# Kernel tuning notes

Hardware: AMD Instinct MI355X
Metric: run time of the kernel (lower is better)

Reference implementation:

```python
import jax, jax.numpy as jnp
import numpy as np

N_NODES = 50000
N_EDGES = 800000
D_IN = 8
D_MODEL = 128
N_CLASSES = 2


def gcn_conv(x, W, b, src, dst, n_nodes):
    # PyG GCNConv: h = x @ W; add self-loops; D^{-1/2} A D^{-1/2} aggregation; + bias
    h = x @ W  # [N, D]
    deg = jax.ops.segment_sum(jnp.ones(src.shape[0], h.dtype), dst, num_segments=n_nodes) + 1.0  # +1 self-loop
    dinv = jax.lax.rsqrt(deg)  # deg >= 1 always
    norm = dinv[src] * dinv[dst]  # [E]
    agg = jax.ops.segment_sum(h[src] * norm[:, None], dst, num_segments=n_nodes)
    agg = agg + h * (dinv * dinv)[:, None]  # self-loop term, norm_ii = dinv_i^2
    return agg + b


def setup_inputs() -> dict:
    key = jax.random.key(0)
    ks = jax.random.split(key, 10)
    x = jax.random.normal(ks[0], (N_NODES, D_IN), jnp.float32)
    edge_index = jax.random.randint(ks[1], (2, N_EDGES), 0, N_NODES, jnp.int64 if jax.config.jax_enable_x64 else jnp.int32)
    def glorot(k, shape):
        lim = np.sqrt(6.0 / (shape[0] + shape[1]))
        return jax.random.uniform(k, shape, jnp.float32, -lim, lim)
    return {
        "x": x,
        "edge_index": edge_index,
        "W1": glorot(ks[2], (D_IN, D_MODEL)),
        "b1": jnp.zeros((D_MODEL,), jnp.float32),
        "W2": glorot(ks[3], (D_MODEL, D_MODEL)),
        "b2": jnp.zeros((D_MODEL,), jnp.float32),
        "Wlin1": glorot(ks[4], (2 * D_MODEL, D_MODEL)),
        "blin1": jnp.zeros((D_MODEL,), jnp.float32),
        "Wfin": glorot(ks[5], (D_MODEL, N_CLASSES)),
        "bfin": jnp.zeros((N_CLASSES,), jnp.float32),
    }


def reference(x, edge_index, W1, b1, W2, b2, Wlin1, blin1, Wfin, bfin):
    src, dst = edge_index[0], edge_index[1]
    n = x.shape[0]
    h = jax.nn.relu(gcn_conv(x, W1, b1, src, dst, n))
    h = jax.nn.relu(gcn_conv(h, W2, b2, src, dst, n))
    xpair = jnp.concatenate((h[src], h[dst]), axis=1)  # [E, 2*D]
    xpair = jax.nn.relu(xpair @ Wlin1 + blin1)
    logits = xpair @ Wfin + bfin  # [E, C]
    return jax.nn.log_softmax(logits, axis=1)
```

## Files before the change

### kernel.cpp

```cpp
#include <hip/hip_runtime.h>
#include <stdint.h>
#include <math.h>

#define D 128

typedef unsigned short u16;
typedef __attribute__((ext_vector_type(8))) short bf16x8;
typedef __attribute__((ext_vector_type(4))) float f32x4;
typedef __attribute__((ext_vector_type(2))) float f32x2;

union BU { uint4 u; bf16x8 s; };

__device__ __forceinline__ unsigned f2bf_pk(float a, float b) {
    union { float f; unsigned u; } x, y; x.f = a; y.f = b;
    unsigned ra = x.u + 0x7FFF + ((x.u >> 16) & 1);
    unsigned rb = y.u + 0x7FFF + ((y.u >> 16) & 1);
    return (ra >> 16) | (rb & 0xFFFF0000u);
}
__device__ __forceinline__ u16 f2bf(float f) {
    union { float f; unsigned u; } x; x.f = f;
    unsigned r = x.u + 0x7FFF + ((x.u >> 16) & 1);
    return (u16)(r >> 16);
}
__device__ __forceinline__ f32x2 bf2f2v(unsigned u) {
    union { unsigned w[2]; f32x2 v; } t;
    t.w[0] = u << 16; t.w[1] = u & 0xFFFF0000u;
    return t.v;
}
__device__ __forceinline__ f32x2 vmax0(f32x2 a) {
    return __builtin_elementwise_max(a, (f32x2)(0.f));
}
__device__ __forceinline__ int padded4(int deg) {
    return (deg + 3) & ~3;
}


__global__ __launch_bounds__(256) void k_degree8(const int* __restrict__ dst, int E,
                                                 int* __restrict__ hist8, int* __restrict__ rank, int N) {
    int i = blockIdx.x * 256 + threadIdx.x;
    int copy = blockIdx.x & 7;
    int E4 = E >> 2;
    if (i < E4) {
        int4 d = ((const int4*)dst)[i];
        int* h = hist8 + copy * N;
        int4 rk;
        rk.x = atomicAdd(&h[d.x], 1);
        rk.y = atomicAdd(&h[d.y], 1);
        rk.z = atomicAdd(&h[d.z], 1);
        rk.w = atomicAdd(&h[d.w], 1);
        ((int4*)rank)[i] = rk;
    }
    if (i == 0) {
        for (int j = E4 * 4; j < E; ++j) rank[j] = atomicAdd(&hist8[dst[j]], 1);
    }
}

__global__ __launch_bounds__(256) void k_xcdoff_bsum(int* __restrict__ hist8, int* __restrict__ degi,
                                                     float* __restrict__ dinv, int* __restrict__ bsum, int N) {
    __shared__ int ws[4];
    int t = threadIdx.x;
    int i = blockIdx.x * 256 + t;
    int pd = 0;
    if (i < N) {
        int run = 0;
#pragma unroll
        for (int j = 0; j < 8; ++j) {
            int c = hist8[j * N + i];
            hist8[j * N + i] = run;
            run += c;
        }
        degi[i] = run;
        dinv[i] = rsqrtf((float)run + 1.0f);
        pd = padded4(run);
    }
    int v = pd;
#pragma unroll
    for (int off = 1; off < 64; off <<= 1) v += __shfl_xor(v, off, 64);
    if ((t & 63) == 0) ws[t >> 6] = v;
    __syncthreads();
    if (t == 0) bsum[blockIdx.x] = ws[0] + ws[1] + ws[2] + ws[3];
}

__global__ __launch_bounds__(1024) void k_boff_wprep(const int* __restrict__ bsum, int* __restrict__ boff,
                                                     int nb, int* __restrict__ prow, int N,
                                                     const float* __restrict__ W2, const float* __restrict__ Wlin,
                                                     unsigned* __restrict__ wswz) {
    int t = threadIdx.x;
    if (blockIdx.x == 0) {
        __shared__ int s[1024];
        s[t] = (t < nb) ? bsum[t] : 0;
        __syncthreads();
        for (int off = 1; off < 1024; off <<= 1) {
            int v = (t >= off) ? s[t - off] : 0;
            __syncthreads();
            s[t] += v;
            __syncthreads();
        }
        if (t < nb) boff[t] = (t == 0) ? 0 : s[t - 1];
        if (t == 0) prow[N] = s[1023];
    } else {
        int tid = (blockIdx.x - 1) * 1024 + t;
        int m = tid >> 13;
        int r = tid & 8191;
        int jp = r & 3;
        int lane = (r >> 2) & 63;
        int ct = (r >> 8) & 7;
        int kc = r >> 11;
        int k0 = kc * 32 + (lane >> 4) * 8 + 2 * jp;
        int n = ct * 16 + (lane & 15);
        const float* srcp = (m == 0) ? W2 : (Wlin + (m - 1) * 16384);
        wswz[tid] = f2bf_pk(srcp[k0 * 128 + n], srcp[(k0 + 1) * 128 + n]);
    }
}

__global__ __launch_bounds__(256) void k_scan_final(const int* __restrict__ degi, const int* __restrict__ boff,
                                                    int* __restrict__ prow, int N, int* __restrict__ hist8) {
    __shared__ int s[256];
    int t = threadIdx.x;
    int i = blockIdx.x * 256 + t;
    int pd = (i < N) ? padded4(degi[i]) : 0;
    s[t] = pd;
    __syncthreads();
    for (int off = 1; off < 256; off <<= 1) {
        int v = (t >= off) ? s[t - off] : 0;
        __syncthreads();
        s[t] += v;
        __syncthreads();
    }
    if (i < N) {
        int p = boff[blockIdx.x] + ((t == 0) ? 0 : s[t - 1]);
        prow[i] = p;
#pragma unroll
        for (int j = 0; j < 8; ++j) hist8[j * N + i] += p;
    }
}


__global__ __launch_bounds__(256) void k_scatter_fill_xform(
        const int* __restrict__ src, const int* __restrict__ dst, int E,
        const int* __restrict__ prow, const int* __restrict__ hist8, const int* __restrict__ rank,
        const int* __restrict__ degi,
        int* __restrict__ colsrc, int N, int eb4, int nb,
        const float* __restrict__ x, const float* __restrict__ W1,
        const float* __restrict__ dinv, unsigned* __restrict__ g) {
    __shared__ float Ws[8 * D];
    int t = threadIdx.x;
    int b = blockIdx.x;
    if (b < eb4) {
        int i = b * 256 + t;
        int copy = b & 7;
        int E4 = E >> 2;
        if (i < E4) {
            int4 d = ((const int4*)dst)[i];
            int4 s4 = ((const int4*)src)[i];
            int4 rk = ((const int4*)rank)[i];
            const int* h = hist8 + copy * N;
            colsrc[h[d.x] + rk.x] = s4.x;
            colsrc[h[d.y] + rk.y] = s4.y;
            colsrc[h[d.z] + rk.z] = s4.z;
            colsrc[h[d.w] + rk.w] = s4.w;
        }
        if (i == 0) {
            for (int j = E4 * 4; j < E; ++j)
                colsrc[hist8[dst[j]] + rank[j]] = src[j];
        }
    } else if (b < eb4 + nb) {
        int n = (b - eb4) * 256 + t;
        if (n < N) {
            int lo = prow[n];
            int deg = degi[n];
            int pd = padded4(deg);
            for (int j = deg; j < pd; ++j) colsrc[lo + j] = N;
        }
        if (b == eb4 && t == 0) {
            int P = prow[N];
            for (int j = 0; j < 16; ++j) colsrc[P + j] = N;
        }
    } else {
        int xb0 = b - eb4 - nb;
        for (int i = t; i < 8 * D; i += 256) Ws[i] = W1[i];
        __syncthreads();
        int node = xb0 * 4 + (t >> 6);
        int l = t & 63;
        if (node < N) {
            float s0 = 0.f, s1 = 0.f;
#pragma unroll
            for (int k = 0; k < 8; ++k) {
                float xv = x[node * 8 + k];
                s0 += xv * Ws[k * D + 2 * l];
                s1 += xv * Ws[k * D + 2 * l + 1];
            }
            float di = dinv[node];
            g[node * 64 + l] = f2bf_pk(s0 * di, s1 * di);
        }
        if (xb0 == 0 && t < 64) g[(size_t)N * 64 + t] = 0;
    }
}


#define HROW 136

template <bool DUAL>
__global__ __launch_bounds__(256) void k_aggemm(const uint4* __restrict__ g, const int* __restrict__ prow,
                                                const int* __restrict__ colsrc, const float* __restrict__ dinv,
                                                const float* __restrict__ biasH,
                                                const uint4* __restrict__ wB0, const uint4* __restrict__ wB1,
                                                const float* __restrict__ bias1,
                                                u16* __restrict__ out0, u16* __restrict__ out1, int N) {
    __shared__ u16 hs[16 * HROW];
    int t = threadIdx.x;
    int wv = t >> 6;
    int lane = t & 63;
    int sub = lane >> 4;
    int r = lane & 15;
    int base = blockIdx.x * 16;

    for (int nd = 0; nd < 4; ++nd) {
        int i = base + wv * 4 + nd;
        int lrow = wv * 4 + nd;
        if (i < N) {
            f32x2 acc2[4];
#pragma unroll
            for (int j = 0; j < 4; ++j) acc2[j] = (f32x2)(0.f);
            int lo = prow[i], hiP = prow[i + 1];
            int idx = lo + sub;
            int c0 = colsrc[idx];
            int c1 = (idx + 4 < hiP) ? colsrc[idx + 4] : N;
            int c2 = (idx + 8 < hiP) ? colsrc[idx + 8] : N;
            uint4 v0 = g[c0 * 16 + r];
            uint4 v1 = g[c1 * 16 + r];
            for (int k = lo; k < hiP; k += 4) {
                int c3 = (idx + 12 < hiP) ? colsrc[idx + 12] : N;
                uint4 v2 = g[c2 * 16 + r];
                acc2[0] += bf2f2v(v0.x);
                acc2[1] += bf2f2v(v0.y);
                acc2[2] += bf2f2v(v0.z);
                acc2[3] += bf2f2v(v0.w);
                v0 = v1; v1 = v2; c2 = c3; idx += 4;
            }
#pragma unroll
            for (int j = 0; j < 4; ++j) {
                acc2[j].x += __shfl_xor(acc2[j].x, 16, 64);
                acc2[j].y += __shfl_xor(acc2[j].y, 16, 64);
                acc2[j].x += __shfl_xor(acc2[j].x, 32, 64);
                acc2[j].y += __shfl_xor(acc2[j].y, 32, 64);
            }
            if (sub == 0) {
                uint4 sv = g[i * 16 + r];
                acc2[0] += bf2f2v(sv.x);
                acc2[1] += bf2f2v(sv.y);
                acc2[2] += bf2f2v(sv.z);
                acc2[3] += bf2f2v(sv.w);
                float di = dinv[i];
                float4 b0 = ((const float4*)biasH)[r * 2];
                float4 b1v = ((const float4*)biasH)[r * 2 + 1];
                float r0 = fmaxf(acc2[0].x * di + b0.x, 0.f);
                float r1 = fmaxf(acc2[0].y * di + b0.y, 0.f);
                float r2 = fmaxf(acc2[1].x * di + b0.z, 0.f);
                float r3 = fmaxf(acc2[1].y * di + b0.w, 0.f);
                float r4 = fmaxf(acc2[2].x * di + b1v.x, 0.f);
                float r5 = fmaxf(acc2[2].y * di + b1v.y, 0.f);
                float r6 = fmaxf(acc2[3].x * di + b1v.z, 0.f);
                float r7 = fmaxf(acc2[3].y * di + b1v.w, 0.f);
                uint4 o;
                o.x = f2bf_pk(r0, r1);
                o.y = f2bf_pk(r2, r3);
                o.z = f2bf_pk(r4, r5);
                o.w = f2bf_pk(r6, r7);
                *(uint4*)(hs + lrow * HROW + r * 8) = o;
            }
        } else if (sub == 0) {
            *(uint4*)(hs + lrow * HROW + r * 8) = make_uint4(0, 0, 0, 0);
        }
    }
    __syncthreads();

    int quad = lane >> 4;
    int l15 = lane & 15;
    int ct0 = wv * 2;

    f32x4 accA[2], accB[2];
#pragma unroll
    for (int q = 0; q < 2; ++q) { accA[q] = (f32x4){0.f, 0.f, 0.f, 0.f}; accB[q] = (f32x4){0.f, 0.f, 0.f, 0.f}; }

    const uint4* hrow = (const uint4*)(hs + l15 * HROW);
#pragma unroll
    for (int kc = 0; kc < 4; ++kc) {
        BU a; a.u = hrow[kc * 4 + quad];
#pragma unroll
        for (int q = 0; q < 2; ++q) {
            BU b0; b0.u = wB0[(kc * 8 + ct0 + q) * 64 + lane];
            accA[q] = __builtin_amdgcn_mfma_f32_16x16x32_bf16(a.s, b0.s, accA[q], 0, 0, 0);
            if (DUAL) {
                BU b1; b1.u = wB1[(kc * 8 + ct0 + q) * 64 + lane];
                accB[q] = __builtin_amdgcn_mfma_f32_16x16x32_bf16(a.s, b1.s, accB[q], 0, 0, 0);
            }
        }
    }
#pragma unroll
    for (int reg = 0; reg < 4; ++reg) {
        int node = base + quad * 4 + reg;
        if (node >= N) continue;
        float sc = DUAL ? 1.0f : dinv[node];
#pragma unroll
        for (int q = 0; q < 2; ++q) {
            int colj = (ct0 + q) * 16 + l15;
            out0[(size_t)node * 128 + colj] = f2bf(accA[q][reg] * sc);
            if (DUAL) out1[(size_t)node * 128 + colj] = f2bf(accB[q][reg] + bias1[colj]);
        }
    }
    if (blockIdx.x == 0 && t < 64) ((unsigned*)out0)[(size_t)N * 64 + t] = 0;
}


__global__ __launch_bounds__(256) void k_edge(const uint4* __restrict__ a, const uint4* __restrict__ c,
                                              const int* __restrict__ src, const int* __restrict__ dst,
                                              const float* __restrict__ Wfin, const float* __restrict__ bfin,
                                              float* __restrict__ out, int E) {
    int t = threadIdx.x;
    int g = t >> 4;
    int r = t & 15;
    int base = blockIdx.x * 64 + g * 4;

    f32x2 wd[4];
    const float4* wvp = (const float4*)Wfin;
#pragma unroll
    for (int q = 0; q < 4; ++q) {
        float4 m = wvp[r * 4 + q];
        wd[q] = (f32x2){m.x - m.y, m.z - m.w};
    }
    float bd = bfin[0] - bfin[1];

    int4 s4, d4;
    if (base + 3 < E) {
        s4 = ((const int4*)src)[blockIdx.x * 16 + g];
        d4 = ((const int4*)dst)[blockIdx.x * 16 + g];
    } else {
        int e0 = base, e1 = base + 1, e2 = base + 2, e3 = base + 3;
        s4.x = (e0 < E) ? src[e0] : 0; d4.x = (e0 < E) ? dst[e0] : 0;
        s4.y = (e1 < E) ? src[e1] : 0; d4.y = (e1 < E) ? dst[e1] : 0;
        s4.z = (e2 < E) ? src[e2] : 0; d4.z = (e2 < E) ? dst[e2] : 0;
        s4.w = (e3 < E) ? src[e3] : 0; d4.w = (e3 < E) ? dst[e3] : 0;
    }

    uint4 av[4], cv[4];
    av[0] = a[(size_t)s4.x * 16 + r];  cv[0] = c[(size_t)d4.x * 16 + r];
    av[1] = a[(size_t)s4.y * 16 + r];  cv[1] = c[(size_t)d4.y * 16 + r];
    av[2] = a[(size_t)s4.z * 16 + r];  cv[2] = c[(size_t)d4.z * 16 + r];
    av[3] = a[(size_t)s4.w * 16 + r];  cv[3] = c[(size_t)d4.w * 16 + r];

    float dl[4];
#pragma unroll
    for (int j = 0; j < 4; ++j) {
        f32x2 p = (f32x2)(0.f);
        f32x2 z;
        z = vmax0(bf2f2v(av[j].x) + bf2f2v(cv[j].x)); p += z * wd[0];
        z = vmax0(bf2f2v(av[j].y) + bf2f2v(cv[j].y)); p += z * wd[1];
        z = vmax0(bf2f2v(av[j].z) + bf2f2v(cv[j].z)); p += z * wd[2];
        z = vmax0(bf2f2v(av[j].w) + bf2f2v(cv[j].w)); p += z * wd[3];
        dl[j] = p.x + p.y;
    }
#pragma unroll
    for (int off = 1; off < 16; off <<= 1) {
#pragma unroll
        for (int j = 0; j < 4; ++j) dl[j] += __shfl_xor(dl[j], off, 64);
    }
    if (r == 0) {
        float o[8];
#pragma unroll
        for (int j = 0; j < 4; ++j) {
            float dlt = dl[j] + bd;
            float tn = -fabsf(dlt);
            float s = __logf(1.f + __expf(tn));
            o[2 * j]     = (dlt >= 0.f) ? -s : (dlt - s);
            o[2 * j + 1] = (dlt >= 0.f) ? (-dlt - s) : -s;
        }
        if (base + 3 < E) {
            float4* op = (float4*)(out + 2 * (size_t)base);
            op[0] = make_float4(o[0], o[1], o[2], o[3]);
            op[1] = make_float4(o[4], o[5], o[6], o[7]);
        } else {
#pragma unroll
            for (int j = 0; j < 4; ++j) {
                if (base + j < E)
                    *((float2*)(out + 2 * (size_t)(base + j))) = make_float2(o[2 * j], o[2 * j + 1]);
            }
        }
    }
}

extern "C" void kernel_launch(void* const* d_in, const int* in_sizes, int n_in,
                              void* d_out, int out_size, void* d_ws, size_t ws_size,
                              hipStream_t stream) {
    const float* x     = (const float*)d_in[0];
    const int*   ei    = (const int*)d_in[1];
    const float* W1    = (const float*)d_in[2];
    const float* b1    = (const float*)d_in[3];
    const float* W2    = (const float*)d_in[4];
    const float* b2    = (const float*)d_in[5];
    const float* Wlin1 = (const float*)d_in[6];
    const float* blin1 = (const float*)d_in[7];
    const float* Wfin  = (const float*)d_in[8];
    const float* bfin  = (const float*)d_in[9];
    float* out = (float*)d_out;

    int N = in_sizes[0] / 8;
    int E = in_sizes[1] / 2;
    const int* src = ei;
    const int* dst = ei + E;
    int nb = (N + 255) / 256;
    int eb4 = (E / 4 + 255) / 256;
    int xb = (N + 3) / 4;

    char* w = (char*)d_ws;
    int* hist8 = (int*)w;     w += (size_t)8 * N * 4;
    int* rank = (int*)w;      w += (size_t)E * 4;
    int* degi = (int*)w;      w += (size_t)N * 4;
    int* prow = (int*)w;      w += (size_t)(N + 1) * 4;
    float* dinv = (float*)w;  w += (size_t)N * 4;
    int* bsum = (int*)w;      w += (size_t)nb * 4;
    int* boff = (int*)w;      w += (size_t)nb * 4;
    w = (char*)(((uintptr_t)w + 255) & ~(uintptr_t)255);
    int* colsrc = (int*)w;    w += ((size_t)E + 8 * (size_t)N + 64) * 4;
    unsigned* wswz = (unsigned*)w; w += (size_t)3 * 8192 * 4;
    unsigned* bufG = (unsigned*)w; w += (size_t)(N + 1) * 64 * 4;
    unsigned* bufA = (unsigned*)w; w += (size_t)(N + 1) * 64 * 4;
    unsigned* bufC = (unsigned*)w; w += (size_t)N * 64 * 4;
    unsigned* bufG2 = (unsigned*)w; w += (size_t)(N + 1) * 64 * 4;

    hipMemsetAsync(hist8, 0, (size_t)8 * N * 4, stream);

    k_degree8<<<eb4, 256, 0, stream>>>(dst, E, hist8, rank, N);
    k_xcdoff_bsum<<<nb, 256, 0, stream>>>(hist8, degi, dinv, bsum, N);
    k_boff_wprep<<<25, 1024, 0, stream>>>(bsum, boff, nb, prow, N, W2, Wlin1, wswz);
    k_scan_final<<<nb, 256, 0, stream>>>(degi, boff, prow, N, hist8);
    k_scatter_fill_xform<<<eb4 + nb + xb, 256, 0, stream>>>(src, dst, E, prow, hist8, rank, degi,
                                                            colsrc, N, eb4, nb, x, W1, dinv, bufG);

    int ablocks = (N + 15) / 16;
    k_aggemm<false><<<ablocks, 256, 0, stream>>>((const uint4*)bufG, prow, colsrc, dinv, b1,
                                                 (const uint4*)wswz, nullptr, nullptr,
                                                 (u16*)bufG2, nullptr, N);
    k_aggemm<true><<<ablocks, 256, 0, stream>>>((const uint4*)bufG2, prow, colsrc, dinv, b2,
                                                (const uint4*)(wswz + 8192), (const uint4*)(wswz + 16384),
                                                blin1, (u16*)bufA, (u16*)bufC, N);

    k_edge<<<(E + 63) / 64, 256, 0, stream>>>((const uint4*)bufA, (const uint4*)bufC,
                                              src, dst, Wfin, bfin, out, E);
}
```

Measured before the change: 273.9 us.

## Aggregate 8-dim raw features before W1 transform in first GCN layer

Layer one now aggregates the dinv-scaled 8-wide input features over neighbors, and only then applies W1, bias and ReLU, followed by the W2 MFMA GEMM in the same kernel. Previously it gathered 128-wide bf16 rows. The prescaled features are written in the degree kernel, and the separate x@W1 transform blocks are dropped from the scatter kernel. This cuts gather traffic in the first aggregation roughly by a factor of eight and keeps the layer-1 math in fp32 before the bf16 cast. The cost is a small per-node 8x128 matmul done on scalar units.

Result: slower. 280.2 us (+2.3%).

```diff
diff --git a/kernel.cpp b/kernel.cpp
--- a/kernel.cpp
+++ b/kernel.cpp
@@ -56,7 +56,8 @@
 }
 
 __global__ __launch_bounds__(256) void k_xcdoff_bsum(int* __restrict__ hist8, int* __restrict__ degi,
-                                                     float* __restrict__ dinv, int* __restrict__ bsum, int N) {
+                                                     float* __restrict__ dinv, int* __restrict__ bsum, int N,
+                                                     const float* __restrict__ x, float* __restrict__ xs) {
     __shared__ int ws[4];
     int t = threadIdx.x;
     int i = blockIdx.x * 256 + t;
@@ -70,8 +71,19 @@
             run += c;
         }
         degi[i] = run;
-        dinv[i] = rsqrtf((float)run + 1.0f);
+        float dv = rsqrtf((float)run + 1.0f);
+        dinv[i] = dv;
+        const float4* xp = (const float4*)(x + (size_t)i * 8);
+        float4 a0 = xp[0], a1 = xp[1];
+        float4 w0 = make_float4(dv * a0.x, dv * a0.y, dv * a0.z, dv * a0.w);
+        float4 w1 = make_float4(dv * a1.x, dv * a1.y, dv * a1.z, dv * a1.w);
+        float4* xo = (float4*)(xs + (size_t)i * 8);
+        xo[0] = w0; xo[1] = w1;
         pd = padded4(run);
+    } else if (i == N) {
+        float4 z = make_float4(0.f, 0.f, 0.f, 0.f);
+        float4* xo = (float4*)(xs + (size_t)N * 8);
+        xo[0] = z; xo[1] = z;
     }
     int v = pd;
 #pragma unroll
@@ -136,21 +148,18 @@
 }
 
 
-__global__ __launch_bounds__(256) void k_scatter_fill_xform(
+__global__ __launch_bounds__(256) void k_scatter_fill(
         const int* __restrict__ src, const int* __restrict__ dst, int E,
         const int* __restrict__ prow, const int* __restrict__ hist8, const int* __restrict__ rank,
         const int* __restrict__ degi,
-        int* __restrict__ colsrc, int N, int eb4, int nb,
-        const float* __restrict__ x, const float* __restrict__ W1,
-        const float* __restrict__ dinv, unsigned* __restrict__ g) {
-    __shared__ float Ws[8 * D];
+        int* __restrict__ colsrc, int N, int eb4) {
     int t = threadIdx.x;
     int b = blockIdx.x;
     if (b < eb4) {
         int i = b * 256 + t;
-        int copy = b & 7;
         int E4 = E >> 2;
         if (i < E4) {
+            int copy = b & 7;
             int4 d = ((const int4*)dst)[i];
             int4 s4 = ((const int4*)src)[i];
             int4 rk = ((const int4*)rank)[i];
@@ -164,7 +173,7 @@
             for (int j = E4 * 4; j < E; ++j)
                 colsrc[hist8[dst[j]] + rank[j]] = src[j];
         }
-    } else if (b < eb4 + nb) {
+    } else {
         int n = (b - eb4) * 256 + t;
         if (n < N) {
             int lo = prow[n];
@@ -176,29 +185,119 @@
             int P = prow[N];
             for (int j = 0; j < 16; ++j) colsrc[P + j] = N;
         }
-    } else {
-        int xb0 = b - eb4 - nb;
-        for (int i = t; i < 8 * D; i += 256) Ws[i] = W1[i];
-        __syncthreads();
-        int node = xb0 * 4 + (t >> 6);
-        int l = t & 63;
-        if (node < N) {
-            float s0 = 0.f, s1 = 0.f;
-#pragma unroll
-            for (int k = 0; k < 8; ++k) {
-                float xv = x[node * 8 + k];
-                s0 += xv * Ws[k * D + 2 * l];
-                s1 += xv * Ws[k * D + 2 * l + 1];
+    }
+}
+
+#define HROW 136
+
+
+__global__ __launch_bounds__(256) void k_agg1gemm(
+        const float* __restrict__ xs, const int* __restrict__ prow,
+        const int* __restrict__ colsrc, const float* __restrict__ dinv,
+        const float* __restrict__ b1, const float* __restrict__ W1,
+        const uint4* __restrict__ wB0, u16* __restrict__ out0, int N) {
+    __shared__ float W1s[8 * 128];
+    __shared__ float b1s[128];
+    __shared__ float ys[16][8];
+    __shared__ u16 hs[16 * HROW];
+    int t = threadIdx.x;
+    int wv = t >> 6;
+    int lane = t & 63;
+    int sub = lane >> 4;
+    int r = lane & 15;
+    int base = blockIdx.x * 16;
+
+    for (int idx = t; idx < 8 * 128; idx += 256) W1s[idx] = W1[idx];
+    if (t < 128) b1s[t] = b1[t];
+
+    int i = base + wv * 4 + sub;
+    if (i < N) {
+        float acc[8];
+#pragma unroll
+        for (int f = 0; f < 8; ++f) acc[f] = 0.f;
+        int lo = prow[i], hiP = prow[i + 1];
+        for (int k = lo + r; k < hiP; k += 16) {
+            int cj = colsrc[k];
+            const float4* xr = (const float4*)(xs + (size_t)cj * 8);
+            float4 u0 = xr[0], u1 = xr[1];
+            acc[0] += u0.x; acc[1] += u0.y; acc[2] += u0.z; acc[3] += u0.w;
+            acc[4] += u1.x; acc[5] += u1.y; acc[6] += u1.z; acc[7] += u1.w;
+        }
+#pragma unroll
+        for (int off = 1; off < 16; off <<= 1) {
+#pragma unroll
+            for (int f = 0; f < 8; ++f) acc[f] += __shfl_xor(acc[f], off, 64);
+        }
+        const float4* xi = (const float4*)(xs + (size_t)i * 8);
+        float4 s0 = xi[0], s1 = xi[1];
+        float di = dinv[i];
+        acc[0] = di * (acc[0] + s0.x); acc[1] = di * (acc[1] + s0.y);
+        acc[2] = di * (acc[2] + s0.z); acc[3] = di * (acc[3] + s0.w);
+        acc[4] = di * (acc[4] + s1.x); acc[5] = di * (acc[5] + s1.y);
+        acc[6] = di * (acc[6] + s1.z); acc[7] = di * (acc[7] + s1.w);
+        if (r < 8) ys[wv * 4 + sub][r] = acc[r];
+    }
+    __syncthreads();
+
+    {
+        int node16 = t >> 4;
+        int cseg = (t & 15) * 8;
+        if (base + node16 < N) {
+            float yv[8];
+#pragma unroll
+            for (int f = 0; f < 8; ++f) yv[f] = ys[node16][f];
+            float o[8];
+#pragma unroll
+            for (int c = 0; c < 8; ++c) {
+                float s = b1s[cseg + c];
+#pragma unroll
+                for (int f = 0; f < 8; ++f) s += yv[f] * W1s[f * 128 + cseg + c];
+                o[c] = fmaxf(s, 0.f);
             }
-            float di = dinv[node];
-            g[node * 64 + l] = f2bf_pk(s0 * di, s1 * di);
-        }
-        if (xb0 == 0 && t < 64) g[(size_t)N * 64 + t] = 0;
-    }
-}
-
-
-#define HROW 136
+            uint4 ov;
+            ov.x = f2bf_pk(o[0], o[1]);
+            ov.y = f2bf_pk(o[2], o[3]);
+            ov.z = f2bf_pk(o[4], o[5]);
+            ov.w = f2bf_pk(o[6], o[7]);
+            *(uint4*)(hs + node16 * HROW + cseg) = ov;
+        } else {
+            *(uint4*)(hs + node16 * HROW + cseg) = make_uint4(0, 0, 0, 0);
+        }
+    }
+    __syncthreads();
+
+    int quad = lane >> 4;
+    int l15 = lane & 15;
+    int ct0 = wv * 2;
+
+    f32x4 accA[2];
+#pragma unroll
+    for (int q = 0; q < 2; ++q) accA[q] = (f32x4){0.f, 0.f, 0.f, 0.f};
+
+    const uint4* hrow = (const uint4*)(hs + l15 * HROW);
+#pragma unroll
+    for (int kc = 0; kc < 4; ++kc) {
+        BU a; a.u = hrow[kc * 4 + quad];
+#pragma unroll
+        for (int q = 0; q < 2; ++q) {
+            BU b0; b0.u = wB0[(kc * 8 + ct0 + q) * 64 + lane];
+            accA[q] = __builtin_amdgcn_mfma_f32_16x16x32_bf16(a.s, b0.s, accA[q], 0, 0, 0);
+        }
+    }
+#pragma unroll
+    for (int reg = 0; reg < 4; ++reg) {
+        int node = base + quad * 4 + reg;
+        if (node >= N) continue;
+        float sc = dinv[node];
+#pragma unroll
+        for (int q = 0; q < 2; ++q) {
+            int colj = (ct0 + q) * 16 + l15;
+            out0[(size_t)node * 128 + colj] = f2bf(accA[q][reg] * sc);
+        }
+    }
+    if (blockIdx.x == 0 && t < 64) ((unsigned*)out0)[(size_t)N * 64 + t] = 0;
+}
+
 
 template <bool DUAL>
 __global__ __launch_bounds__(256) void k_aggemm(const uint4* __restrict__ g, const int* __restrict__ prow,
@@ -410,7 +509,6 @@
     const int* dst = ei + E;
     int nb = (N + 255) / 256;
     int eb4 = (E / 4 + 255) / 256;
-    int xb = (N + 3) / 4;
 
     char* w = (char*)d_ws;
     int* hist8 = (int*)w;     w += (size_t)8 * N * 4;
@@ -423,7 +521,7 @@
     w = (char*)(((uintptr_t)w + 255) & ~(uintptr_t)255);
     int* colsrc = (int*)w;    w += ((size_t)E + 8 * (size_t)N + 64) * 4;
     unsigned* wswz = (unsigned*)w; w += (size_t)3 * 8192 * 4;
-    unsigned* bufG = (unsigned*)w; w += (size_t)(N + 1) * 64 * 4;
+    float* xs = (float*)w;    w += (size_t)(N + 1) * 8 * 4;
     unsigned* bufA = (unsigned*)w; w += (size_t)(N + 1) * 64 * 4;
     unsigned* bufC = (unsigned*)w; w += (size_t)N * 64 * 4;
     unsigned* bufG2 = (unsigned*)w; w += (size_t)(N + 1) * 64 * 4;
@@ -431,16 +529,15 @@
     hipMemsetAsync(hist8, 0, (size_t)8 * N * 4, stream);
 
     k_degree8<<<eb4, 256, 0, stream>>>(dst, E, hist8, rank, N);
-    k_xcdoff_bsum<<<nb, 256, 0, stream>>>(hist8, degi, dinv, bsum, N);
+    k_xcdoff_bsum<<<nb, 256, 0, stream>>>(hist8, degi, dinv, bsum, N, x, xs);
     k_boff_wprep<<<25, 1024, 0, stream>>>(bsum, boff, nb, prow, N, W2, Wlin1, wswz);
     k_scan_final<<<nb, 256, 0, stream>>>(degi, boff, prow, N, hist8);
-    k_scatter_fill_xform<<<eb4 + nb + xb, 256, 0, stream>>>(src, dst, E, prow, hist8, rank, degi,
-                                                            colsrc, N, eb4, nb, x, W1, dinv, bufG);
+    k_scatter_fill<<<eb4 + nb, 256, 0, stream>>>(src, dst, E, prow, hist8, rank, degi,
+                                                 colsrc, N, eb4);
 
     int ablocks = (N + 15) / 16;
-    k_aggemm<false><<<ablocks, 256, 0, stream>>>((const uint4*)bufG, prow, colsrc, dinv, b1,
-                                                 (const uint4*)wswz, nullptr, nullptr,
-                                                 (u16*)bufG2, nullptr, N);
+    k_agg1gemm<<<ablocks, 256, 0, stream>>>(xs, prow, colsrc, dinv, b1, W1,
+                                            (const uint4*)wswz, (u16*)bufG2, N);
     k_aggemm<true><<<ablocks, 256, 0, stream>>>((const uint4*)bufG2, prow, colsrc, dinv, b2,
                                                 (const uint4*)(wswz + 8192), (const uint4*)(wswz + 16384),
                                                 blin1, (u16*)bufA, (u16*)bufC, N);
```
